# Optimization experiments

Measured on AMD Instinct MI355X. Metric: run time of the kernel, lower is better.

The kernel has to match this reference:

```python
import jax, jax.numpy as jnp
import numpy as np

N_ATOMS = 100000
M_NBR = 12
ATOM_F = 64
NBR_F = 41
BN_EPS = 1e-5


def setup_inputs() -> dict:
    key = jax.random.key(0)
    ks = jax.random.split(key, 6)
    atom_in_fea = jax.random.normal(ks[0], (N_ATOMS, ATOM_F), dtype=jnp.float32)
    nbr_fea = jax.random.normal(ks[1], (N_ATOMS, M_NBR, NBR_F), dtype=jnp.float32)
    nbr_fea_idx = jax.random.randint(ks[2], (N_ATOMS, M_NBR), 0, N_ATOMS)
    in_dim = 2 * ATOM_F + NBR_F  # 169
    out_dim = 2 * ATOM_F  # 128
    # torch nn.Linear init scale
    bound = 1.0 / np.sqrt(in_dim)
    fc_w = jax.random.uniform(ks[3], (out_dim, in_dim), minval=-bound, maxval=bound, dtype=jnp.float32)
    fc_b = jax.random.uniform(ks[4], (out_dim,), minval=-bound, maxval=bound, dtype=jnp.float32)
    return {
        "atom_in_fea": atom_in_fea,
        "nbr_fea": nbr_fea,
        "nbr_fea_idx": nbr_fea_idx,
        "fc_w": fc_w,
        "fc_b": fc_b,
        "bn1_gamma": jnp.ones((out_dim,), jnp.float32),
        "bn1_beta": jnp.zeros((out_dim,), jnp.float32),
        "bn2_gamma": jnp.ones((ATOM_F,), jnp.float32),
        "bn2_beta": jnp.zeros((ATOM_F,), jnp.float32),
    }


def _batchnorm(x, gamma, beta):
    # training-mode BN (torch default): biased batch statistics over axis 0
    mean = x.mean(axis=0)
    var = x.var(axis=0)
    return (x - mean) * jax.lax.rsqrt(var + BN_EPS) * gamma + beta


def reference(atom_in_fea, nbr_fea, nbr_fea_idx, fc_w, fc_b,
              bn1_gamma, bn1_beta, bn2_gamma, bn2_beta):
    N, M = nbr_fea_idx.shape
    F = atom_in_fea.shape[1]
    atom_nbr_fea = atom_in_fea[nbr_fea_idx]                      # [N, M, F] gather
    self_fea = jnp.broadcast_to(atom_in_fea[:, None, :], (N, M, F))
    total_nbr_fea = jnp.concatenate([self_fea, atom_nbr_fea, nbr_fea], axis=2)  # [N, M, 2F+E]
    gated = jnp.einsum('nmi,oi->nmo', total_nbr_fea, fc_w) + fc_b               # [N, M, 2F]
    gated = _batchnorm(gated.reshape(-1, 2 * F), bn1_gamma, bn1_beta).reshape(N, M, 2 * F)
    nbr_filter = jax.nn.sigmoid(gated[..., :F])
    nbr_core = jax.nn.softplus(gated[..., F:])
    nbr_sumed = jnp.sum(nbr_filter * nbr_core, axis=1)           # [N, F]
    nbr_sumed = _batchnorm(nbr_sumed, bn2_gamma, bn2_beta)
    return jax.nn.softplus(atom_in_fea + nbr_sumed)
```

## Files before the change

kernel.cpp:

```cpp
#include <hip/hip_runtime.h>
#include <stdint.h>

typedef __attribute__((ext_vector_type(8))) short bf16x8;
typedef __attribute__((ext_vector_type(4))) float f32x4;

static constexpr int MNBR   = 12;
static constexpr int AF     = 64;
static constexpr int EF     = 41;
static constexpr int IN_DIM = 2 * AF + EF;
static constexpr float BN_EPS = 1e-5f;

static constexpr int EW_ROW_U16 = 132;

__device__ __forceinline__ uint16_t f2bfbits(float f) {
    uint32_t x = __float_as_uint(f);
    uint32_t r = x + 0x7fffu + ((x >> 16) & 1u);
    return (uint16_t)(r >> 16);
}
__device__ __forceinline__ float softplusf(float x) {
    return fmaxf(x, 0.f) + __logf(1.0f + __expf(-fabsf(x)));
}

__global__ __launch_bounds__(256) void k_prep(
    const float* __restrict__ fc_w, uint16_t* __restrict__ wp_proj,
    uint16_t* __restrict__ wp_edge)
{
    int e = blockIdx.x * 256 + threadIdx.x;
    if (e < 16384) {
        int j = e & 7, lane = (e >> 3) & 63, s = (e >> 9) & 1, t = e >> 10;
        int n = lane & 15, q = lane >> 4;
        int k = s * 32 + q * 8 + j;
        int c = t * 16 + n;
        float v = (c < 128) ? fc_w[c * IN_DIM + k]
                            : fc_w[(c - 128) * IN_DIM + 64 + k];
        wp_proj[e] = f2bfbits(v);
    } else if (e < 24576) {
        int e2 = e - 16384;
        int j = e2 & 7, lane = (e2 >> 3) & 63, s = (e2 >> 9) & 1, t = e2 >> 10;
        int n = lane & 15, q = lane >> 4;
        int k = s * 32 + q * 8 + j;
        int o = t * 16 + n;
        wp_edge[e2] = (k < EF) ? f2bfbits(fc_w[o * IN_DIM + 2 * AF + k])
                               : (uint16_t)0;
    }
}

__global__ __launch_bounds__(256) void k_proj(
    const float* __restrict__ atom_in, const uint16_t* __restrict__ wp_proj,
    const float* __restrict__ fc_b, uint32_t* __restrict__ Ps32,
    uint32_t* __restrict__ Pn32, int N)
{
    const int lane = threadIdx.x & 63;
    const int w    = __builtin_amdgcn_readfirstlane((int)(threadIdx.x >> 6));
    const int a0   = blockIdx.x * 64 + w * 16;
    const int mrow = lane & 15, q = lane >> 4;
    const int arow = a0 + mrow;

    bf16x8 A0 = {}, A1 = {};
    if (arow < N) {
        const float* pa = atom_in + (size_t)arow * AF;
#pragma unroll
        for (int j = 0; j < 8; ++j) {
            A0[j] = (short)f2bfbits(pa[q * 8 + j]);
            A1[j] = (short)f2bfbits(pa[32 + q * 8 + j]);
        }
    }

    const bf16x8* wp = (const bf16x8*)wp_proj;
#pragma unroll
    for (int t = 0; t < 4; ++t) {
        bf16x8 f0 = wp[((t    ) * 2 + 0) * 64 + lane];
        bf16x8 f1 = wp[((t    ) * 2 + 1) * 64 + lane];
        bf16x8 c0 = wp[((t + 4) * 2 + 0) * 64 + lane];
        bf16x8 c1 = wp[((t + 4) * 2 + 1) * 64 + lane];
        f32x4 af = {0.f, 0.f, 0.f, 0.f}, ac = {0.f, 0.f, 0.f, 0.f};
        af = __builtin_amdgcn_mfma_f32_16x16x32_bf16(A0, f0, af, 0, 0, 0);
        af = __builtin_amdgcn_mfma_f32_16x16x32_bf16(A1, f1, af, 0, 0, 0);
        ac = __builtin_amdgcn_mfma_f32_16x16x32_bf16(A0, c0, ac, 0, 0, 0);
        ac = __builtin_amdgcn_mfma_f32_16x16x32_bf16(A1, c1, ac, 0, 0, 0);
        const int oo = t * 16 + (lane & 15);
        const float bf_ = fc_b[oo], bc_ = fc_b[64 + oo];
#pragma unroll
        for (int r = 0; r < 4; ++r) {
            const int atom = a0 + q * 4 + r;
            if (atom < N) {
                const uint32_t lo = f2bfbits(af[r] + bf_);
                const uint32_t hi = f2bfbits(ac[r] + bc_);
                Ps32[(size_t)atom * 64 + oo] = lo | (hi << 16);
            }
        }
    }
#pragma unroll
    for (int t = 0; t < 4; ++t) {
        bf16x8 f0 = wp[((t +  8) * 2 + 0) * 64 + lane];
        bf16x8 f1 = wp[((t +  8) * 2 + 1) * 64 + lane];
        bf16x8 c0 = wp[((t + 12) * 2 + 0) * 64 + lane];
        bf16x8 c1 = wp[((t + 12) * 2 + 1) * 64 + lane];
        f32x4 af = {0.f, 0.f, 0.f, 0.f}, ac = {0.f, 0.f, 0.f, 0.f};
        af = __builtin_amdgcn_mfma_f32_16x16x32_bf16(A0, f0, af, 0, 0, 0);
        af = __builtin_amdgcn_mfma_f32_16x16x32_bf16(A1, f1, af, 0, 0, 0);
        ac = __builtin_amdgcn_mfma_f32_16x16x32_bf16(A0, c0, ac, 0, 0, 0);
        ac = __builtin_amdgcn_mfma_f32_16x16x32_bf16(A1, c1, ac, 0, 0, 0);
        const int oo = t * 16 + (lane & 15);
#pragma unroll
        for (int r = 0; r < 4; ++r) {
            const int atom = a0 + q * 4 + r;
            if (atom < N) {
                const uint32_t lo = f2bfbits(af[r]);
                const uint32_t hi = f2bfbits(ac[r]);
                Pn32[(size_t)atom * 64 + oo] = lo | (hi << 16);
            }
        }
    }
}

template <int MODE>
__global__ __launch_bounds__(256) void k_conv(
    const uint32_t* __restrict__ Ps32, const uint32_t* __restrict__ Pn32,
    const float* __restrict__ nbr, const int* __restrict__ idx,
    const uint16_t* __restrict__ wp_edge, const float* __restrict__ bn1coef,
    float* __restrict__ partial, float* __restrict__ nsum, int N)
{
    __shared__ uint16_t ew16[2][4][16 * EW_ROW_U16];
    __shared__ float red[4][256];
    __shared__ uint16_t bsh[8192];

    const int tid  = threadIdx.x;
    const int lane = tid & 63;
    const int w    = __builtin_amdgcn_readfirstlane((int)(tid >> 6));
    const int col  = lane & 15, q = lane >> 4;
    const int o    = lane;
    (void)N;

    const int rbase = blockIdx.x * 384 + w * 96;
    const int nbase = rbase / 12;

    int idxA = idx[rbase + lane];
    int idxB = 0;
    if (lane < 32) idxB = idx[rbase + 64 + lane];

    {
        const uint4* s4 = (const uint4*)wp_edge;
        uint4* d4 = (uint4*)bsh;
#pragma unroll
        for (int k = 0; k < 4; ++k) d4[k * 256 + tid] = s4[k * 256 + tid];
    }

    float s1f = 0.f, h1f = 0.f, s1c = 0.f, h1c = 0.f;
    if (MODE == 1) {
        s1f = bn1coef[o];       h1f = bn1coef[128 + o];
        s1c = bn1coef[64 + o];  h1c = bn1coef[192 + o];
    }

    float sA = 0.f, qA = 0.f, sB = 0.f, qB = 0.f;
    float accm = 0.f, psf = 0.f, psc = 0.f;
    const bf16x8* bvs = (const bf16x8*)bsh;

    f32x4 e0_A, e1_A, e2_A, e3_A; float e4_A;
    f32x4 e0_B, e1_B, e2_B, e3_B; float e4_B;
    uint32_t ps0_A, ps1_A, ps0_B, ps1_B;
    uint32_t pnA0, pnA1, pnA2,  pnA3,  pnA4,  pnA5,  pnA6,  pnA7;
    uint32_t pnA8, pnA9, pnA10, pnA11, pnA12, pnA13, pnA14, pnA15;
    uint32_t pnB0, pnB1, pnB2,  pnB3,  pnB4,  pnB5,  pnB6,  pnB7;
    uint32_t pnB8, pnB9, pnB10, pnB11, pnB12, pnB13, pnB14, pnB15;

#define GATH(mt, S, i)                                                        \
    {                                                                         \
        const int g_ = (mt) * 16 + (i);                                       \
        const int j_ = (g_ < 64) ? __builtin_amdgcn_readlane(idxA, g_)        \
                                 : __builtin_amdgcn_readlane(idxB, g_ - 64);  \
        pn##S##i = Pn32[(size_t)j_ * 64 + o];                                 \
    }

#define ISSUE(mt, S)                                                          \
    {                                                                         \
        const float* er_ = nbr + (size_t)(rbase + (mt) * 16 + col) * EF;      \
        __builtin_memcpy(&e0_##S, er_ + q * 8, 16);                           \
        __builtin_memcpy(&e1_##S, er_ + q * 8 + 4, 16);                       \
        e4_##S = 0.f;                                                         \
        if (q == 0) {                                                         \
            __builtin_memcpy(&e2_##S, er_ + 32, 16);                          \
            __builtin_memcpy(&e3_##S, er_ + 36, 16);                          \
        } else if (q == 1) {                                                  \
            e4_##S = er_[40];                                                 \
        }                                                                     \
        const int aA_ = ((mt) * 16 + 11) / 12;                                \
        ps0_##S = 0u; ps1_##S = 0u;                                           \
        if (aA_ * 12 < (mt) * 16 + 16)                                        \
            ps0_##S = Ps32[(size_t)(nbase + aA_) * 64 + o];                   \
        if (aA_ * 12 + 12 < (mt) * 16 + 16)                                   \
            ps1_##S = Ps32[(size_t)(nbase + aA_ + 1) * 64 + o];               \
    }                                                                         \
    GATH(mt, S, 0)  GATH(mt, S, 1)  GATH(mt, S, 2)  GATH(mt, S, 3)            \
    GATH(mt, S, 4)  GATH(mt, S, 5)  GATH(mt, S, 6)  GATH(mt, S, 7)            \
    GATH(mt, S, 8)  GATH(mt, S, 9)  GATH(mt, S, 10) GATH(mt, S, 11)           \
    GATH(mt, S, 12) GATH(mt, S, 13) GATH(mt, S, 14) GATH(mt, S, 15)

#define COMPUTE(mt, S)                                                        \
    {                                                                         \
        bf16x8 A0_, A1_ = {};                                                 \
        _Pragma("unroll")                                                     \
        for (int j = 0; j < 4; ++j) {                                         \
            A0_[j]     = (short)f2bfbits(e0_##S[j]);                          \
            A0_[4 + j] = (short)f2bfbits(e1_##S[j]);                          \
        }                                                                     \
        if (q == 0) {                                                         \
            _Pragma("unroll")                                                 \
            for (int j = 0; j < 4; ++j) {                                     \
                A1_[j]     = (short)f2bfbits(e2_##S[j]);                      \
                A1_[4 + j] = (short)f2bfbits(e3_##S[j]);                      \
            }                                                                 \
        } else if (q == 1) {                                                  \
            A1_[0] = (short)f2bfbits(e4_##S);                                 \
        }                                                                     \
        uint16_t* dst_ = &ew16[(mt) & 1][w][0];                               \
        _Pragma("unroll")                                                     \
        for (int t = 0; t < 8; ++t) {                                         \
            bf16x8 b0_ = bvs[(t * 2 + 0) * 64 + lane];                        \
            bf16x8 b1_ = bvs[(t * 2 + 1) * 64 + lane];                        \
            f32x4 a_ = {0.f, 0.f, 0.f, 0.f};                                  \
            a_ = __builtin_amdgcn_mfma_f32_16x16x32_bf16(A0_, b0_, a_, 0, 0, 0); \
            a_ = __builtin_amdgcn_mfma_f32_16x16x32_bf16(A1_, b1_, a_, 0, 0, 0); \
            const int ch_  = t * 16 + col;                                    \
            const int pos_ = (ch_ < 64) ? (ch_ * 2) : ((ch_ - 64) * 2 + 1);   \
            _Pragma("unroll")                                                 \
            for (int r = 0; r < 4; ++r)                                       \
                dst_[(q * 4 + r) * EW_ROW_U16 + pos_] = f2bfbits(a_[r]);      \
        }                                                                     \
    }

#define EPIROW(mt, i, PN)                                                     \
    {                                                                         \
        constexpr int g_ = (mt) * 16 + (i);                                   \
        constexpr int m_ = g_ % 12;                                           \
        if (m_ == 0) {                                                        \
            const uint32_t pp_ = useB_ ? ps1v_ : ps0v_;                       \
            useB_ = true;                                                     \
            psf  = __uint_as_float(pp_ << 16);                                \
            psc  = __uint_as_float(pp_ & 0xffff0000u);                        \
            accm = 0.f;                                                       \
        }                                                                     \
        uint32_t pr_;                                                         \
        __builtin_memcpy(&pr_, &myew_[(i) * EW_ROW_U16 + 2 * o], 4);          \
        const float ewf = __uint_as_float(pr_ << 16);                         \
        const float ewc = __uint_as_float(pr_ & 0xffff0000u);                 \
        const float pnf = __uint_as_float((PN) << 16);                        \
        const float pnc = __uint_as_float((PN) & 0xffff0000u);                \
        const float gf = ewf + psf + pnf;                                     \
        const float gc = ewc + psc + pnc;                                     \
        if (MODE == 0) {                                                      \
            sA += gf; qA = fmaf(gf, gf, qA);                                  \
            sB += gc; qB = fmaf(gc, gc, qB);                                  \
        } else {                                                              \
            const float xf = fmaf(gf, s1f, h1f);                              \
            const float xc = fmaf(gc, s1c, h1c);                              \
            const float filt = 1.0f / (1.0f + __expf(-xf));                   \
            accm = fmaf(filt, softplusf(xc), accm);                           \
            if (m_ == 11) {                                                   \
                nsum[(size_t)(nbase + g_ / 12) * AF + o] = accm;              \
                sB += accm; qB = fmaf(accm, accm, qB);                        \
            }                                                                 \
        }                                                                     \
    }

#define EPILOG(mt, S)                                                         \
    {                                                                         \
        const uint16_t* myew_ = &ew16[(mt) & 1][w][0];                        \
        const uint32_t ps0v_ = ps0_##S, ps1v_ = ps1_##S;                      \
        bool useB_ = false;                                                   \
        EPIROW(mt, 0,  pn##S##0)  EPIROW(mt, 1,  pn##S##1)                    \
        EPIROW(mt, 2,  pn##S##2)  EPIROW(mt, 3,  pn##S##3)                    \
        EPIROW(mt, 4,  pn##S##4)  EPIROW(mt, 5,  pn##S##5)                    \
        EPIROW(mt, 6,  pn##S##6)  EPIROW(mt, 7,  pn##S##7)                    \
        EPIROW(mt, 8,  pn##S##8)  EPIROW(mt, 9,  pn##S##9)                    \
        EPIROW(mt, 10, pn##S##10) EPIROW(mt, 11, pn##S##11)                   \
        EPIROW(mt, 12, pn##S##12) EPIROW(mt, 13, pn##S##13)                   \
        EPIROW(mt, 14, pn##S##14) EPIROW(mt, 15, pn##S##15)                   \
    }

    __syncthreads();

    ISSUE(0, A)
    COMPUTE(0, A)
    __syncthreads();
    ISSUE(1, B)  EPILOG(0, A)
    COMPUTE(1, B)
    __syncthreads();
    ISSUE(2, A)  EPILOG(1, B)
    COMPUTE(2, A)
    __syncthreads();
    ISSUE(3, B)  EPILOG(2, A)
    COMPUTE(3, B)
    __syncthreads();
    ISSUE(4, A)  EPILOG(3, B)
    COMPUTE(4, A)
    __syncthreads();
    ISSUE(5, B)  EPILOG(4, A)
    COMPUTE(5, B)
    __syncthreads();
    EPILOG(5, B)

#undef GATH
#undef ISSUE
#undef COMPUTE
#undef EPIROW
#undef EPILOG

    if (MODE == 0) {
        red[w][0 * 64 + lane] = sA;
        red[w][1 * 64 + lane] = qA;
        red[w][2 * 64 + lane] = sB;
        red[w][3 * 64 + lane] = qB;
        __syncthreads();
        const int s = threadIdx.x;
        const int oc = (s & 127) >> 1;
        const int v  = (s >> 7) * 2 + (s & 1);
        const int mp = v * 64 + oc;
        partial[(size_t)blockIdx.x * 256 + s] =
            red[0][mp] + red[1][mp] + red[2][mp] + red[3][mp];
    } else {
        red[w][0 * 64 + lane] = sB;
        red[w][1 * 64 + lane] = qB;
        __syncthreads();
        const int s = threadIdx.x;
        if (s < 128) {
            const int oc = s >> 1;
            const int v  = s & 1;
            const int mp = v * 64 + oc;
            partial[(size_t)blockIdx.x * 128 + s] =
                red[0][mp] + red[1][mp] + red[2][mp] + red[3][mp];
        }
    }
}

__global__ __launch_bounds__(256) void k_bn_fin(
    const float* __restrict__ partial, const float* __restrict__ gamma,
    const float* __restrict__ beta, float* __restrict__ coef,
    int nch, int NB, float invR)
{
    const int c = blockIdx.x;
    const int tid = threadIdx.x;
    float s = 0.f, qq = 0.f;
    for (int i = tid; i < NB; i += 256) {
        const float* pp = partial + (size_t)i * (2 * nch) + 2 * c;
        s += pp[0]; qq += pp[1];
    }
    __shared__ float ls[256], lq[256];
    ls[tid] = s; lq[tid] = qq;
    __syncthreads();
    for (int off = 128; off > 0; off >>= 1) {
        if (tid < off) { ls[tid] += ls[tid + off]; lq[tid] += lq[tid + off]; }
        __syncthreads();
    }
    if (tid == 0) {
        float mean = ls[0] * invR;
        float var  = fmaxf(lq[0] * invR - mean * mean, 0.f);
        float sc = gamma[c] * rsqrtf(var + BN_EPS);
        coef[c]       = sc;
        coef[nch + c] = beta[c] - mean * sc;
    }
}

__global__ __launch_bounds__(256) void k_final(
    const float* __restrict__ atom_in, const float* __restrict__ nsum,
    const float* __restrict__ bn2, float* __restrict__ out, int total)
{
    int i = blockIdx.x * 256 + threadIdx.x;
    if (i >= total) return;
    int f = i & (AF - 1);
    float v = fmaf(nsum[i], bn2[f], bn2[AF + f]);
    float x = atom_in[i] + v;
    out[i] = softplusf(x);
}

extern "C" void kernel_launch(void* const* d_in, const int* in_sizes, int n_in,
                              void* d_out, int out_size, void* d_ws, size_t ws_size,
                              hipStream_t stream)
{
    const float* atom_in = (const float*)d_in[0];
    const float* nbr_fea = (const float*)d_in[1];
    const int*   nbr_idx = (const int*)d_in[2];
    const float* fc_w    = (const float*)d_in[3];
    const float* fc_b    = (const float*)d_in[4];
    const float* g1      = (const float*)d_in[5];
    const float* b1      = (const float*)d_in[6];
    const float* g2      = (const float*)d_in[7];
    const float* b2      = (const float*)d_in[8];
    float* out = (float*)d_out;

    const int N = in_sizes[0] / AF;
    const int conv_blocks = N / 32;
    const int NB = conv_blocks;

    char* ws = (char*)d_ws;
    size_t off = 0;
    uint16_t* wp_proj = (uint16_t*)(ws + off); off += 16384 * 2;
    uint16_t* wp_edge = (uint16_t*)(ws + off); off += 8192 * 2;
    uint16_t* Ps = (uint16_t*)(ws + off); off += (size_t)N * 128 * 2;
    uint16_t* Pn = (uint16_t*)(ws + off); off += (size_t)N * 128 * 2;
    float* bn1  = (float*)(ws + off);  off += 256 * 4;
    float* bn2c = (float*)(ws + off);  off += 128 * 4;
    off = (off + 511) & ~(size_t)511;
    float* nsum = (float*)(ws + off);
    float* p1   = nsum;
    off += (size_t)N * AF * 4;
    float* p2   = (float*)(ws + off);  off += (size_t)NB * 128 * 4;

    k_prep<<<96, 256, 0, stream>>>(fc_w, wp_proj, wp_edge);
    k_proj<<<(N + 63) / 64, 256, 0, stream>>>(atom_in, wp_proj, fc_b,
                                              (uint32_t*)Ps, (uint32_t*)Pn, N);
    k_conv<0><<<conv_blocks, 256, 0, stream>>>((const uint32_t*)Ps,
                                               (const uint32_t*)Pn,
                                               nbr_fea, nbr_idx, wp_edge,
                                               nullptr, p1, nullptr, N);
    k_bn_fin<<<128, 256, 0, stream>>>(p1, g1, b1, bn1, 128, NB,
                                      1.0f / (float)(N * MNBR));
    k_conv<1><<<conv_blocks, 256, 0, stream>>>((const uint32_t*)Ps,
                                               (const uint32_t*)Pn,
                                               nbr_fea, nbr_idx, wp_edge,
                                               bn1, p2, nsum, N);
    k_bn_fin<<<64, 256, 0, stream>>>(p2, g2, b2, bn2c, 64, NB, 1.0f / (float)N);

    const int total = N * AF;
    k_final<<<(total + 255) / 256, 256, 0, stream>>>(atom_in, nsum, bn2c, out,
                                                     total);
}
```

Before: 632.6 us.

## Replace block barriers and double-buffered tiles with per-wave LDS fence in conv kernel

Each wave only reads back its own region of the edge-projection LDS buffer, so the block-wide __syncthreads between tiles is replaced by a wave-local lgkmcnt wait plus scheduling barriers. The double-buffered A/B register and LDS sets are collapsed into one buffer, and tiles now run strictly issue→compute→epilogue. This drops barrier stalls and halves register and LDS use, which may raise occupancy. The cost is that gather loads for the next tile no longer overlap with the current tile's epilogue, and the sched_barriers block the compiler from interleaving work.

```diff
diff --git a/kernel.cpp b/kernel.cpp
--- a/kernel.cpp
+++ b/kernel.cpp
@@ -19,6 +19,11 @@
 }
 __device__ __forceinline__ float softplusf(float x) {
     return fmaxf(x, 0.f) + __logf(1.0f + __expf(-fabsf(x)));
+}
+
+__device__ __forceinline__ void wave_lds_fence() {
+    asm volatile("s_waitcnt lgkmcnt(0)" ::: "memory");
+    __builtin_amdgcn_sched_barrier(0);
 }
 
 __global__ __launch_bounds__(256) void k_prep(
@@ -121,7 +126,7 @@
     const uint16_t* __restrict__ wp_edge, const float* __restrict__ bn1coef,
     float* __restrict__ partial, float* __restrict__ nsum, int N)
 {
-    __shared__ uint16_t ew16[2][4][16 * EW_ROW_U16];
+    __shared__ uint16_t ew16[4][16 * EW_ROW_U16];
     __shared__ float red[4][256];
     __shared__ uint16_t bsh[8192];
 
@@ -154,66 +159,64 @@
 
     float sA = 0.f, qA = 0.f, sB = 0.f, qB = 0.f;
     float accm = 0.f, psf = 0.f, psc = 0.f;
+    uint16_t* myew = ew16[w];
     const bf16x8* bvs = (const bf16x8*)bsh;
 
-    f32x4 e0_A, e1_A, e2_A, e3_A; float e4_A;
-    f32x4 e0_B, e1_B, e2_B, e3_B; float e4_B;
-    uint32_t ps0_A, ps1_A, ps0_B, ps1_B;
-    uint32_t pnA0, pnA1, pnA2,  pnA3,  pnA4,  pnA5,  pnA6,  pnA7;
-    uint32_t pnA8, pnA9, pnA10, pnA11, pnA12, pnA13, pnA14, pnA15;
-    uint32_t pnB0, pnB1, pnB2,  pnB3,  pnB4,  pnB5,  pnB6,  pnB7;
-    uint32_t pnB8, pnB9, pnB10, pnB11, pnB12, pnB13, pnB14, pnB15;
-
-#define GATH(mt, S, i)                                                        \
+    f32x4 e0, e1, e2 = {0.f, 0.f, 0.f, 0.f}, e3 = {0.f, 0.f, 0.f, 0.f};
+    float e4;
+    uint32_t ps0, ps1;
+    uint32_t pn0, pn1, pn2,  pn3,  pn4,  pn5,  pn6,  pn7;
+    uint32_t pn8, pn9, pn10, pn11, pn12, pn13, pn14, pn15;
+
+#define GATH(mt, i)                                                           \
     {                                                                         \
         const int g_ = (mt) * 16 + (i);                                       \
         const int j_ = (g_ < 64) ? __builtin_amdgcn_readlane(idxA, g_)        \
                                  : __builtin_amdgcn_readlane(idxB, g_ - 64);  \
-        pn##S##i = Pn32[(size_t)j_ * 64 + o];                                 \
-    }
-
-#define ISSUE(mt, S)                                                          \
+        pn##i = Pn32[(size_t)j_ * 64 + o];                                    \
+    }
+
+#define ISSUE(mt)                                                             \
     {                                                                         \
         const float* er_ = nbr + (size_t)(rbase + (mt) * 16 + col) * EF;      \
-        __builtin_memcpy(&e0_##S, er_ + q * 8, 16);                           \
-        __builtin_memcpy(&e1_##S, er_ + q * 8 + 4, 16);                       \
-        e4_##S = 0.f;                                                         \
+        __builtin_memcpy(&e0, er_ + q * 8, 16);                               \
+        __builtin_memcpy(&e1, er_ + q * 8 + 4, 16);                           \
+        e4 = 0.f;                                                             \
         if (q == 0) {                                                         \
-            __builtin_memcpy(&e2_##S, er_ + 32, 16);                          \
-            __builtin_memcpy(&e3_##S, er_ + 36, 16);                          \
+            __builtin_memcpy(&e2, er_ + 32, 16);                              \
+            __builtin_memcpy(&e3, er_ + 36, 16);                              \
         } else if (q == 1) {                                                  \
-            e4_##S = er_[40];                                                 \
+            e4 = er_[40];                                                     \
         }                                                                     \
         const int aA_ = ((mt) * 16 + 11) / 12;                                \
-        ps0_##S = 0u; ps1_##S = 0u;                                           \
+        ps0 = 0u; ps1 = 0u;                                                   \
         if (aA_ * 12 < (mt) * 16 + 16)                                        \
-            ps0_##S = Ps32[(size_t)(nbase + aA_) * 64 + o];                   \
+            ps0 = Ps32[(size_t)(nbase + aA_) * 64 + o];                       \
         if (aA_ * 12 + 12 < (mt) * 16 + 16)                                   \
-            ps1_##S = Ps32[(size_t)(nbase + aA_ + 1) * 64 + o];               \
+            ps1 = Ps32[(size_t)(nbase + aA_ + 1) * 64 + o];                   \
     }                                                                         \
-    GATH(mt, S, 0)  GATH(mt, S, 1)  GATH(mt, S, 2)  GATH(mt, S, 3)            \
-    GATH(mt, S, 4)  GATH(mt, S, 5)  GATH(mt, S, 6)  GATH(mt, S, 7)            \
-    GATH(mt, S, 8)  GATH(mt, S, 9)  GATH(mt, S, 10) GATH(mt, S, 11)           \
-    GATH(mt, S, 12) GATH(mt, S, 13) GATH(mt, S, 14) GATH(mt, S, 15)
-
-#define COMPUTE(mt, S)                                                        \
+    GATH(mt, 0)  GATH(mt, 1)  GATH(mt, 2)  GATH(mt, 3)                        \
+    GATH(mt, 4)  GATH(mt, 5)  GATH(mt, 6)  GATH(mt, 7)                        \
+    GATH(mt, 8)  GATH(mt, 9)  GATH(mt, 10) GATH(mt, 11)                       \
+    GATH(mt, 12) GATH(mt, 13) GATH(mt, 14) GATH(mt, 15)
+
+#define COMPUTE(mt)                                                           \
     {                                                                         \
         bf16x8 A0_, A1_ = {};                                                 \
         _Pragma("unroll")                                                     \
         for (int j = 0; j < 4; ++j) {                                         \
-            A0_[j]     = (short)f2bfbits(e0_##S[j]);                          \
-            A0_[4 + j] = (short)f2bfbits(e1_##S[j]);                          \
+            A0_[j]     = (short)f2bfbits(e0[j]);                              \
+            A0_[4 + j] = (short)f2bfbits(e1[j]);                              \
         }                                                                     \
         if (q == 0) {                                                         \
             _Pragma("unroll")                                                 \
             for (int j = 0; j < 4; ++j) {                                     \
-                A1_[j]     = (short)f2bfbits(e2_##S[j]);                      \
-                A1_[4 + j] = (short)f2bfbits(e3_##S[j]);                      \
+                A1_[j]     = (short)f2bfbits(e2[j]);                          \
+                A1_[4 + j] = (short)f2bfbits(e3[j]);                          \
             }                                                                 \
         } else if (q == 1) {                                                  \
-            A1_[0] = (short)f2bfbits(e4_##S);                                 \
-        }                                                                     \
-        uint16_t* dst_ = &ew16[(mt) & 1][w][0];                               \
+            A1_[0] = (short)f2bfbits(e4);                                     \
+        }                                                                     \
         _Pragma("unroll")                                                     \
         for (int t = 0; t < 8; ++t) {                                         \
             bf16x8 b0_ = bvs[(t * 2 + 0) * 64 + lane];                        \
@@ -225,7 +228,7 @@
             const int pos_ = (ch_ < 64) ? (ch_ * 2) : ((ch_ - 64) * 2 + 1);   \
             _Pragma("unroll")                                                 \
             for (int r = 0; r < 4; ++r)                                       \
-                dst_[(q * 4 + r) * EW_ROW_U16 + pos_] = f2bfbits(a_[r]);      \
+                myew[(q * 4 + r) * EW_ROW_U16 + pos_] = f2bfbits(a_[r]);      \
         }                                                                     \
     }
 
@@ -234,14 +237,14 @@
         constexpr int g_ = (mt) * 16 + (i);                                   \
         constexpr int m_ = g_ % 12;                                           \
         if (m_ == 0) {                                                        \
-            const uint32_t pp_ = useB_ ? ps1v_ : ps0v_;                       \
+            const uint32_t pp_ = useB_ ? ps1 : ps0;                           \
             useB_ = true;                                                     \
             psf  = __uint_as_float(pp_ << 16);                                \
             psc  = __uint_as_float(pp_ & 0xffff0000u);                        \
             accm = 0.f;                                                       \
         }                                                                     \
         uint32_t pr_;                                                         \
-        __builtin_memcpy(&pr_, &myew_[(i) * EW_ROW_U16 + 2 * o], 4);          \
+        __builtin_memcpy(&pr_, &myew[(i) * EW_ROW_U16 + 2 * o], 4);           \
         const float ewf = __uint_as_float(pr_ << 16);                         \
         const float ewc = __uint_as_float(pr_ & 0xffff0000u);                 \
         const float pnf = __uint_as_float((PN) << 16);                        \
@@ -263,48 +266,36 @@
         }                                                                     \
     }
 
-#define EPILOG(mt, S)                                                         \
+#define EPILOG(mt)                                                            \
     {                                                                         \
-        const uint16_t* myew_ = &ew16[(mt) & 1][w][0];                        \
-        const uint32_t ps0v_ = ps0_##S, ps1v_ = ps1_##S;                      \
         bool useB_ = false;                                                   \
-        EPIROW(mt, 0,  pn##S##0)  EPIROW(mt, 1,  pn##S##1)                    \
-        EPIROW(mt, 2,  pn##S##2)  EPIROW(mt, 3,  pn##S##3)                    \
-        EPIROW(mt, 4,  pn##S##4)  EPIROW(mt, 5,  pn##S##5)                    \
-        EPIROW(mt, 6,  pn##S##6)  EPIROW(mt, 7,  pn##S##7)                    \
-        EPIROW(mt, 8,  pn##S##8)  EPIROW(mt, 9,  pn##S##9)                    \
-        EPIROW(mt, 10, pn##S##10) EPIROW(mt, 11, pn##S##11)                   \
-        EPIROW(mt, 12, pn##S##12) EPIROW(mt, 13, pn##S##13)                   \
-        EPIROW(mt, 14, pn##S##14) EPIROW(mt, 15, pn##S##15)                   \
-    }
+        EPIROW(mt, 0,  pn0)  EPIROW(mt, 1,  pn1)                              \
+        EPIROW(mt, 2,  pn2)  EPIROW(mt, 3,  pn3)                              \
+        EPIROW(mt, 4,  pn4)  EPIROW(mt, 5,  pn5)                              \
+        EPIROW(mt, 6,  pn6)  EPIROW(mt, 7,  pn7)                              \
+        EPIROW(mt, 8,  pn8)  EPIROW(mt, 9,  pn9)                              \
+        EPIROW(mt, 10, pn10) EPIROW(mt, 11, pn11)                             \
+        EPIROW(mt, 12, pn12) EPIROW(mt, 13, pn13)                             \
+        EPIROW(mt, 14, pn14) EPIROW(mt, 15, pn15)                             \
+    }
+
+#define TILE(mt)                                                              \
+    ISSUE(mt)                                                                 \
+    COMPUTE(mt)                                                               \
+    wave_lds_fence();                                                         \
+    EPILOG(mt)                                                                \
+    __builtin_amdgcn_sched_barrier(0);
 
     __syncthreads();
 
-    ISSUE(0, A)
-    COMPUTE(0, A)
-    __syncthreads();
-    ISSUE(1, B)  EPILOG(0, A)
-    COMPUTE(1, B)
-    __syncthreads();
-    ISSUE(2, A)  EPILOG(1, B)
-    COMPUTE(2, A)
-    __syncthreads();
-    ISSUE(3, B)  EPILOG(2, A)
-    COMPUTE(3, B)
-    __syncthreads();
-    ISSUE(4, A)  EPILOG(3, B)
-    COMPUTE(4, A)
-    __syncthreads();
-    ISSUE(5, B)  EPILOG(4, A)
-    COMPUTE(5, B)
-    __syncthreads();
-    EPILOG(5, B)
+    TILE(0) TILE(1) TILE(2) TILE(3) TILE(4) TILE(5)
 
 #undef GATH
 #undef ISSUE
 #undef COMPUTE
 #undef EPIROW
 #undef EPILOG
+#undef TILE
 
     if (MODE == 0) {
         red[w][0 * 64 + lane] = sA;
```

Measured after the change: 598.9 us. 5.3% less time.

## Replace block barriers with per-wave LDS fences and pair MFMA tiles for packed stores

Applied to the files above, without the earlier changes.

Each wave's edge-projection staging buffer is private, so the block-wide __syncthreads between compute and epilogue are replaced with a per-wave lgkmcnt wait plus scheduling barriers. The staging buffer drops from double to single buffering. Loads are issued one tile further ahead, so a tile's gather is in flight while the previous tile is computed. The MFMA loop now computes the filter and core halves together and writes them as one packed 32-bit LDS store instead of separate 16-bit stores. This removes cross-wave stalls and halves the LDS store count, but it raises register pressure from holding two tiles of prefetched loads at once.

```diff
diff --git a/kernel.cpp b/kernel.cpp
--- a/kernel.cpp
+++ b/kernel.cpp
@@ -19,6 +19,11 @@
 }
 __device__ __forceinline__ float softplusf(float x) {
     return fmaxf(x, 0.f) + __logf(1.0f + __expf(-fabsf(x)));
+}
+
+__device__ __forceinline__ void wave_lds_fence() {
+    asm volatile("s_waitcnt lgkmcnt(0)" ::: "memory");
+    __builtin_amdgcn_sched_barrier(0);
 }
 
 __global__ __launch_bounds__(256) void k_prep(
@@ -121,7 +126,7 @@
     const uint16_t* __restrict__ wp_edge, const float* __restrict__ bn1coef,
     float* __restrict__ partial, float* __restrict__ nsum, int N)
 {
-    __shared__ uint16_t ew16[2][4][16 * EW_ROW_U16];
+    __shared__ uint16_t ew16[4][16 * EW_ROW_U16];
     __shared__ float red[4][256];
     __shared__ uint16_t bsh[8192];
 
@@ -154,10 +159,12 @@
 
     float sA = 0.f, qA = 0.f, sB = 0.f, qB = 0.f;
     float accm = 0.f, psf = 0.f, psc = 0.f;
+    uint16_t* myew = ew16[w];
     const bf16x8* bvs = (const bf16x8*)bsh;
 
-    f32x4 e0_A, e1_A, e2_A, e3_A; float e4_A;
-    f32x4 e0_B, e1_B, e2_B, e3_B; float e4_B;
+    f32x4 e0_A, e1_A, e2_A = {0.f,0.f,0.f,0.f}, e3_A = {0.f,0.f,0.f,0.f};
+    f32x4 e0_B, e1_B, e2_B = {0.f,0.f,0.f,0.f}, e3_B = {0.f,0.f,0.f,0.f};
+    float e4_A, e4_B;
     uint32_t ps0_A, ps1_A, ps0_B, ps1_B;
     uint32_t pnA0, pnA1, pnA2,  pnA3,  pnA4,  pnA5,  pnA6,  pnA7;
     uint32_t pnA8, pnA9, pnA10, pnA11, pnA12, pnA13, pnA14, pnA15;
@@ -213,39 +220,45 @@
         } else if (q == 1) {                                                  \
             A1_[0] = (short)f2bfbits(e4_##S);                                 \
         }                                                                     \
-        uint16_t* dst_ = &ew16[(mt) & 1][w][0];                               \
         _Pragma("unroll")                                                     \
-        for (int t = 0; t < 8; ++t) {                                         \
-            bf16x8 b0_ = bvs[(t * 2 + 0) * 64 + lane];                        \
-            bf16x8 b1_ = bvs[(t * 2 + 1) * 64 + lane];                        \
-            f32x4 a_ = {0.f, 0.f, 0.f, 0.f};                                  \
-            a_ = __builtin_amdgcn_mfma_f32_16x16x32_bf16(A0_, b0_, a_, 0, 0, 0); \
-            a_ = __builtin_amdgcn_mfma_f32_16x16x32_bf16(A1_, b1_, a_, 0, 0, 0); \
-            const int ch_  = t * 16 + col;                                    \
-            const int pos_ = (ch_ < 64) ? (ch_ * 2) : ((ch_ - 64) * 2 + 1);   \
+        for (int t = 0; t < 4; ++t) {                                         \
+            bf16x8 b0lo = bvs[((t    ) * 2 + 0) * 64 + lane];                 \
+            bf16x8 b1lo = bvs[((t    ) * 2 + 1) * 64 + lane];                 \
+            bf16x8 b0hi = bvs[((t + 4) * 2 + 0) * 64 + lane];                 \
+            bf16x8 b1hi = bvs[((t + 4) * 2 + 1) * 64 + lane];                 \
+            f32x4 alo = {0.f, 0.f, 0.f, 0.f}, ahi = {0.f, 0.f, 0.f, 0.f};     \
+            alo = __builtin_amdgcn_mfma_f32_16x16x32_bf16(A0_, b0lo, alo, 0, 0, 0); \
+            alo = __builtin_amdgcn_mfma_f32_16x16x32_bf16(A1_, b1lo, alo, 0, 0, 0); \
+            ahi = __builtin_amdgcn_mfma_f32_16x16x32_bf16(A0_, b0hi, ahi, 0, 0, 0); \
+            ahi = __builtin_amdgcn_mfma_f32_16x16x32_bf16(A1_, b1hi, ahi, 0, 0, 0); \
+            const int cc = t * 16 + col;                                      \
             _Pragma("unroll")                                                 \
-            for (int r = 0; r < 4; ++r)                                       \
-                dst_[(q * 4 + r) * EW_ROW_U16 + pos_] = f2bfbits(a_[r]);      \
-        }                                                                     \
-    }
-
-#define EPIROW(mt, i, PN)                                                     \
+            for (int r = 0; r < 4; ++r) {                                     \
+                const uint32_t pk = (uint32_t)f2bfbits(alo[r])                \
+                                  | ((uint32_t)f2bfbits(ahi[r]) << 16);       \
+                __builtin_memcpy(&myew[(q * 4 + r) * EW_ROW_U16 + 2 * cc],    \
+                                 &pk, 4);                                     \
+            }                                                                 \
+        }                                                                     \
+    }
+
+#define EPIROW(mt, S, i)                                                      \
     {                                                                         \
         constexpr int g_ = (mt) * 16 + (i);                                   \
         constexpr int m_ = g_ % 12;                                           \
         if (m_ == 0) {                                                        \
-            const uint32_t pp_ = useB_ ? ps1v_ : ps0v_;                       \
+            const uint32_t pp_ = useB_ ? ps1_##S : ps0_##S;                   \
             useB_ = true;                                                     \
             psf  = __uint_as_float(pp_ << 16);                                \
             psc  = __uint_as_float(pp_ & 0xffff0000u);                        \
             accm = 0.f;                                                       \
         }                                                                     \
         uint32_t pr_;                                                         \
-        __builtin_memcpy(&pr_, &myew_[(i) * EW_ROW_U16 + 2 * o], 4);          \
+        __builtin_memcpy(&pr_, &myew[(i) * EW_ROW_U16 + 2 * o], 4);           \
         const float ewf = __uint_as_float(pr_ << 16);                         \
         const float ewc = __uint_as_float(pr_ & 0xffff0000u);                 \
-        const float pnf = __uint_as_float((PN) << 16);                        \
-        const float pnc = __uint_as_float((PN) & 0xffff0000u);                \
+        const float pnf = __uint_as_float(pn##S##i << 16);                    \
+        const float pnc = __uint_as_float(pn##S##i & 0xffff0000u);            \
         const float gf = ewf + psf + pnf;                                     \
         const float gc = ewc + psc + pnc;                                     \
         if (MODE == 0) {                                                      \
@@ -265,40 +278,34 @@
 
 #define EPILOG(mt, S)                                                         \
     {                                                                         \
-        const uint16_t* myew_ = &ew16[(mt) & 1][w][0];                        \
-        const uint32_t ps0v_ = ps0_##S, ps1v_ = ps1_##S;                      \
         bool useB_ = false;                                                   \
-        EPIROW(mt, 0,  pn##S##0)  EPIROW(mt, 1,  pn##S##1)                    \
-        EPIROW(mt, 2,  pn##S##2)  EPIROW(mt, 3,  pn##S##3)                    \
-        EPIROW(mt, 4,  pn##S##4)  EPIROW(mt, 5,  pn##S##5)                    \
-        EPIROW(mt, 6,  pn##S##6)  EPIROW(mt, 7,  pn##S##7)                    \
-        EPIROW(mt, 8,  pn##S##8)  EPIROW(mt, 9,  pn##S##9)                    \
-        EPIROW(mt, 10, pn##S##10) EPIROW(mt, 11, pn##S##11)                   \
-        EPIROW(mt, 12, pn##S##12) EPIROW(mt, 13, pn##S##13)                   \
-        EPIROW(mt, 14, pn##S##14) EPIROW(mt, 15, pn##S##15)                   \
+        EPIROW(mt, S, 0)  EPIROW(mt, S, 1)  EPIROW(mt, S, 2)                  \
+        EPIROW(mt, S, 3)  EPIROW(mt, S, 4)  EPIROW(mt, S, 5)                  \
+        EPIROW(mt, S, 6)  EPIROW(mt, S, 7)  EPIROW(mt, S, 8)                  \
+        EPIROW(mt, S, 9)  EPIROW(mt, S, 10) EPIROW(mt, S, 11)                 \
+        EPIROW(mt, S, 12) EPIROW(mt, S, 13) EPIROW(mt, S, 14)                 \
+        EPIROW(mt, S, 15)                                                     \
     }
 
     __syncthreads();
 
     ISSUE(0, A)
-    COMPUTE(0, A)
-    __syncthreads();
-    ISSUE(1, B)  EPILOG(0, A)
-    COMPUTE(1, B)
-    __syncthreads();
-    ISSUE(2, A)  EPILOG(1, B)
-    COMPUTE(2, A)
-    __syncthreads();
-    ISSUE(3, B)  EPILOG(2, A)
-    COMPUTE(3, B)
-    __syncthreads();
-    ISSUE(4, A)  EPILOG(3, B)
-    COMPUTE(4, A)
-    __syncthreads();
-    ISSUE(5, B)  EPILOG(4, A)
-    COMPUTE(5, B)
-    __syncthreads();
-    EPILOG(5, B)
+    ISSUE(1, B)
+    COMPUTE(0, A)  wave_lds_fence();  EPILOG(0, A)
+    __builtin_amdgcn_sched_barrier(0);
+    ISSUE(2, A)
+    COMPUTE(1, B)  wave_lds_fence();  EPILOG(1, B)
+    __builtin_amdgcn_sched_barrier(0);
+    ISSUE(3, B)
+    COMPUTE(2, A)  wave_lds_fence();  EPILOG(2, A)
+    __builtin_amdgcn_sched_barrier(0);
+    ISSUE(4, A)
+    COMPUTE(3, B)  wave_lds_fence();  EPILOG(3, B)
+    __builtin_amdgcn_sched_barrier(0);
+    ISSUE(5, B)
+    COMPUTE(4, A)  wave_lds_fence();  EPILOG(4, A)
+    __builtin_amdgcn_sched_barrier(0);
+    COMPUTE(5, B)  wave_lds_fence();  EPILOG(5, B)
 
 #undef GATH
 #undef ISSUE
```

Result: faster. 601.6 us (-4.9%).
